# Kernel optimization log

Hardware: AMD Instinct MI355X
Metric: run time of the kernel (lower is better)

## Reference

```python
import jax, jax.numpy as jnp
import numpy as np

B, T, C = 2, 4096, 768
N_HEAD = 12
HEAD_DIM = C // N_HEAD


def setup_inputs() -> dict:
    key = jax.random.key(0)
    k1, k2, k3, k4, k5 = jax.random.split(key, 5)
    scale = 1.0 / np.sqrt(C)
    x = jax.random.normal(k1, (B, T, C), dtype=jnp.float32)
    # weights stored as [in, out] (transpose of torch Linear weight)
    W_attn = jax.random.normal(k2, (C, 3 * C), dtype=jnp.float32) * scale
    b_attn = jax.random.normal(k3, (3 * C,), dtype=jnp.float32) * 0.01
    W_proj = jax.random.normal(k4, (C, C), dtype=jnp.float32) * scale
    b_proj = jax.random.normal(k5, (C,), dtype=jnp.float32) * 0.01
    return {"x": x, "W_attn": W_attn, "b_attn": b_attn, "W_proj": W_proj, "b_proj": b_proj}


def reference(x, W_attn, b_attn, W_proj, b_proj):
    Bq, Tq, Cq = x.shape
    qkv = x @ W_attn + b_attn                      # [B, T, 3C]
    q, k, v = jnp.split(qkv, 3, axis=-1)           # each [B, T, C]

    def heads(t):
        return t.reshape(Bq, Tq, N_HEAD, HEAD_DIM).transpose(0, 2, 1, 3)  # [B, H, T, D]

    q, k, v = heads(q), heads(k), heads(v)
    att = jnp.einsum('bhqd,bhkd->bhqk', q, k) * (1.0 / np.sqrt(HEAD_DIM))  # [B, H, T, T]
    causal = jnp.tril(jnp.ones((Tq, Tq), dtype=bool))                      # [T, T]
    att = jnp.where(causal[None, None], att, jnp.finfo(att.dtype).min)
    att = jax.nn.softmax(att, axis=-1)
    y = jnp.einsum('bhqk,bhkd->bhqd', att, v)      # [B, H, T, D]
    y = y.transpose(0, 2, 1, 3).reshape(Bq, Tq, Cq)
    return y @ W_proj + b_proj
```

## Files before the change

### kernel.cpp

```cpp
#include <hip/hip_runtime.h>


#define TSEQ   4096
#define NHEAD  12
#define CDIM   768
#define C3     2304
#define BT_TOT 8192

#define PSTR   72

typedef __bf16 bf16x8 __attribute__((ext_vector_type(8)));
typedef float  f32x4  __attribute__((ext_vector_type(4)));

__device__ __forceinline__ unsigned short f2bf(float f) {
  unsigned int u = __builtin_bit_cast(unsigned int, f);
  u += 0x7FFFu + ((u >> 16) & 1u);
  return (unsigned short)(u >> 16);
}

__device__ __forceinline__ unsigned int pack2bf(float a, float b) {
  return (unsigned int)f2bf(a) | ((unsigned int)f2bf(b) << 16);
}

__device__ __forceinline__ f32x4 mfma16(bf16x8 a, bf16x8 b, f32x4 c) {
  return __builtin_amdgcn_mfma_f32_16x16x32_bf16(a, b, c, 0, 0, 0);
}

typedef const __attribute__((address_space(1))) void* gas_ptr;
typedef __attribute__((address_space(3))) void* las_ptr;

#define LGKM_WAIT() __builtin_amdgcn_s_waitcnt(0xC07F)


__global__ __launch_bounds__(256) void cast_f32_bf16(const float* __restrict__ x,
                                                     unsigned short* __restrict__ o, int n) {
  int i = (blockIdx.x * 256 + threadIdx.x) * 4;
  if (i < n) {
    float4 v = *(const float4*)(x + i);
    ushort4 u;
    u.x = f2bf(v.x); u.y = f2bf(v.y); u.z = f2bf(v.z); u.w = f2bf(v.w);
    *(ushort4*)(o + i) = u;
  }
}

__global__ __launch_bounds__(256) void transpose_cast(const float* __restrict__ src,
                                                      unsigned short* __restrict__ dst,
                                                      int K, int N) {
  __shared__ float tile[32][33];
  int n0 = blockIdx.x * 32, k0 = blockIdx.y * 32;
  int tx = threadIdx.x, ty = threadIdx.y;
#pragma unroll
  for (int i = 0; i < 4; ++i)
    tile[ty + i * 8][tx] = src[(size_t)(k0 + ty + i * 8) * N + n0 + tx];
  __syncthreads();
#pragma unroll
  for (int i = 0; i < 4; ++i)
    dst[(size_t)(n0 + ty + i * 8) * K + k0 + tx] = f2bf(tile[tx][ty + i * 8]);
}


__device__ __forceinline__ void gemm_bt_mainloop(const unsigned short* __restrict__ A,
                                                 const unsigned short* __restrict__ BTm,
                                                 int K, int m0, int n0,
                                                 unsigned short* lds, f32x4 acc[4][4]) {
  const int tid = threadIdx.x;
  const int wave = tid >> 6, lane = tid & 63;
  const int quad = lane >> 4, l16 = lane & 15;
  const int wm = (wave >> 1) * 64, wn = (wave & 1) * 64;
  const int srow = tid >> 2;
  const int scol = (tid & 3) * 8;

  for (int k0 = 0; k0 < K; k0 += 32) {
    __syncthreads();
#pragma unroll
    for (int r = 0; r < 2; ++r) {
      const unsigned short* ga = A + (size_t)(m0 + r * 64 + srow) * K + k0 + scol;
      __builtin_amdgcn_global_load_lds((gas_ptr)ga,
          (las_ptr)(lds + r * 2048 + wave * 512), 16, 0, 0);
      const unsigned short* gb = BTm + (size_t)(n0 + r * 64 + srow) * K + k0 + scol;
      __builtin_amdgcn_global_load_lds((gas_ptr)gb,
          (las_ptr)(lds + 4096 + r * 2048 + wave * 512), 16, 0, 0);
    }
    __syncthreads();

    bf16x8 af[4], bfr[4];
#pragma unroll
    for (int i = 0; i < 4; ++i) {
      af[i]  = *(const bf16x8*)(lds + (wm + i * 16 + l16) * 32 + quad * 8);
      bfr[i] = *(const bf16x8*)(lds + 4096 + (wn + i * 16 + l16) * 32 + quad * 8);
    }
#pragma unroll
    for (int i = 0; i < 4; ++i)
#pragma unroll
      for (int j = 0; j < 4; ++j)
        acc[i][j] = mfma16(af[i], bfr[j], acc[i][j]);
  }
}

__global__ __launch_bounds__(256) void gemm_qkv_kernel(
    const unsigned short* __restrict__ A, const unsigned short* __restrict__ BTm,
    const float* __restrict__ bias,
    unsigned short* __restrict__ qbuf, unsigned short* __restrict__ kbuf,
    unsigned short* __restrict__ vtbuf) {
  __shared__ __align__(16) unsigned short lds[8192];
  f32x4 zero = {0.f, 0.f, 0.f, 0.f};
  f32x4 acc[4][4];
#pragma unroll
  for (int i = 0; i < 4; ++i)
#pragma unroll
    for (int j = 0; j < 4; ++j) acc[i][j] = zero;

  const int m0 = blockIdx.y * 128, n0 = blockIdx.x * 128;
  gemm_bt_mainloop(A, BTm, CDIM, m0, n0, lds, acc);

  const int tid = threadIdx.x;
  const int wave = tid >> 6, lane = tid & 63;
  const int quad = lane >> 4, l16 = lane & 15;
  const int wm = (wave >> 1) * 64, wn = (wave & 1) * 64;
  const float KSCALE = 0.125f * 1.44269504088896340736f;

#pragma unroll
  for (int j = 0; j < 4; ++j) {
    int n = n0 + wn + j * 16 + l16;
    float bv = bias[n];
    int seg = n / CDIM;
    int nn = n - seg * CDIM;
    int h = nn >> 6, d = nn & 63;
    float mult = (seg == 1) ? KSCALE : 1.0f;
#pragma unroll
    for (int i = 0; i < 4; ++i) {
#pragma unroll
      for (int r = 0; r < 4; ++r) {
        int m = m0 + wm + i * 16 + quad * 4 + r;
        int b = m >> 12, t = m & (TSEQ - 1);
        unsigned short val = f2bf((acc[i][j][r] + bv) * mult);
        size_t bh = (size_t)(b * NHEAD + h);
        if (seg == 0)      qbuf[(bh * TSEQ + t) * 64 + d] = val;
        else if (seg == 1) kbuf[(bh * TSEQ + t) * 64 + d] = val;
        else               vtbuf[(bh * 64 + d) * TSEQ + t] = val;
      }
    }
  }
}

__global__ __launch_bounds__(256) void gemm_out_kernel(
    const unsigned short* __restrict__ A, const unsigned short* __restrict__ BTm,
    const float* __restrict__ bias, float* __restrict__ out) {
  __shared__ __align__(16) unsigned short lds[8192];
  f32x4 zero = {0.f, 0.f, 0.f, 0.f};
  f32x4 acc[4][4];
#pragma unroll
  for (int i = 0; i < 4; ++i)
#pragma unroll
    for (int j = 0; j < 4; ++j) acc[i][j] = zero;

  const int m0 = blockIdx.y * 128, n0 = blockIdx.x * 128;
  gemm_bt_mainloop(A, BTm, CDIM, m0, n0, lds, acc);

  const int tid = threadIdx.x;
  const int wave = tid >> 6, lane = tid & 63;
  const int quad = lane >> 4, l16 = lane & 15;
  const int wm = (wave >> 1) * 64, wn = (wave & 1) * 64;

#pragma unroll
  for (int j = 0; j < 4; ++j) {
    int n = n0 + wn + j * 16 + l16;
    float bv = bias[n];
#pragma unroll
    for (int i = 0; i < 4; ++i) {
#pragma unroll
      for (int r = 0; r < 4; ++r) {
        int m = m0 + wm + i * 16 + quad * 4 + r;
        out[(size_t)m * CDIM + n] = acc[i][j][r] + bv;
      }
    }
  }
}


__device__ __forceinline__ void stage_kv4(const unsigned short* __restrict__ Kp,
                                          const unsigned short* __restrict__ Vp,
                                          int j0, unsigned short* kb, unsigned short* vb,
                                          int tid, int wave) {
  const int row = tid >> 3;
  const int col = ((tid & 7) ^ (row & 7)) * 8;
  __builtin_amdgcn_global_load_lds((gas_ptr)(Kp + (size_t)(j0 + row) * 64 + col),
                                   (las_ptr)(kb + wave * 512), 16, 0, 0);
  __builtin_amdgcn_global_load_lds((gas_ptr)(Kp + (size_t)(j0 + 32 + row) * 64 + col),
                                   (las_ptr)(kb + 2048 + wave * 512), 16, 0, 0);
  __builtin_amdgcn_global_load_lds((gas_ptr)(Vp + (size_t)row * TSEQ + j0 + col),
                                   (las_ptr)(vb + wave * 512), 16, 0, 0);
  __builtin_amdgcn_global_load_lds((gas_ptr)(Vp + (size_t)(row + 32) * TSEQ + j0 + col),
                                   (las_ptr)(vb + 2048 + wave * 512), 16, 0, 0);
}

__device__ __forceinline__ void qk_score(const bf16x8 kf[8], const bf16x8 qf[2], f32x4 s[4]) {
  f32x4 zero = {0.f, 0.f, 0.f, 0.f};
#pragma unroll
  for (int i = 0; i < 4; ++i)
    s[i] = mfma16(kf[2 * i + 1], qf[1], mfma16(kf[2 * i], qf[0], zero));
}

template <bool MASKED>
__device__ __forceinline__ void exp_write(const f32x4 s[4], unsigned short* __restrict__ prow,
                                          int j0, int q0, int l16, int quad, float& lsum) {
#pragma unroll
  for (int i = 0; i < 4; ++i) {
    float p[4];
#pragma unroll
    for (int r = 0; r < 4; ++r) {
      p[r] = __builtin_amdgcn_exp2f(s[i][r]);
      if (MASKED) {
        if (j0 + i * 16 + quad * 4 + r > q0 + l16) p[r] = 0.f;
      }
      lsum += p[r];
    }
    uint2 w;
    w.x = pack2bf(p[0], p[1]);
    w.y = pack2bf(p[2], p[3]);
    *(uint2*)(prow + l16 * PSTR + i * 16 + quad * 4) = w;
  }
}

__global__ __launch_bounds__(256) void attn_kernel(const unsigned short* __restrict__ qbuf,
                                                   const unsigned short* __restrict__ kbuf,
                                                   const unsigned short* __restrict__ vtbuf,
                                                   unsigned short* __restrict__ y) {
  __shared__ __align__(16) unsigned short k_lds[2][64 * 64];
  __shared__ __align__(16) unsigned short v_lds[2][64 * 64];
  __shared__ __align__(16) unsigned short p_lds[4][16 * PSTR];

  const int tid = threadIdx.x;
  const int wave = tid >> 6, lane = tid & 63;
  const int quad = lane >> 4, l16 = lane & 15;

  const int bh = blockIdx.x % 24;
  const int qtile = 63 - (blockIdx.x / 24);
  const int q0 = qtile * 64 + wave * 16;

  const unsigned short* Qp = qbuf + (size_t)bh * TSEQ * 64;
  const unsigned short* Kp = kbuf + (size_t)bh * TSEQ * 64;
  const unsigned short* Vp = vtbuf + (size_t)bh * 64 * TSEQ;
  unsigned short* prow = &p_lds[wave][0];

  bf16x8 qf[2];
  qf[0] = *(const bf16x8*)(Qp + (size_t)(q0 + l16) * 64 + quad * 8);
  qf[1] = *(const bf16x8*)(Qp + (size_t)(q0 + l16) * 64 + 32 + quad * 8);

  f32x4 zero = {0.f, 0.f, 0.f, 0.f};
  f32x4 o[4];
#pragma unroll
  for (int dt = 0; dt < 4; ++dt) o[dt] = zero;
  float lsum = 0.f;

  const int kcol0 = (quad ^ (l16 & 7)) * 8;
  const int ntiles = qtile + 1;

  stage_kv4(Kp, Vp, 0, k_lds[0], v_lds[0], tid, wave);

  for (int jt = 0; jt < ntiles; ++jt) {
    __syncthreads();
    if (jt + 1 < ntiles)
      stage_kv4(Kp, Vp, (jt + 1) * 64, k_lds[(jt + 1) & 1], v_lds[(jt + 1) & 1], tid, wave);

    const unsigned short* kb = k_lds[jt & 1];
    const unsigned short* vb = v_lds[jt & 1];

    bf16x8 kf[8];
#pragma unroll
    for (int i = 0; i < 4; ++i) {
      kf[2 * i]     = *(const bf16x8*)(kb + (16 * i + l16) * 64 + kcol0);
      kf[2 * i + 1] = *(const bf16x8*)(kb + (16 * i + l16) * 64 + (kcol0 ^ 32));
    }
    f32x4 s[4];
    qk_score(kf, qf, s);

    if (jt == qtile) exp_write<true>(s, prow, jt * 64, q0, l16, quad, lsum);
    else             exp_write<false>(s, prow, jt * 64, q0, l16, quad, lsum);

    LGKM_WAIT();
    bf16x8 pf0 = *(const bf16x8*)(prow + l16 * PSTR + quad * 8);
    bf16x8 pf1 = *(const bf16x8*)(prow + l16 * PSTR + 32 + quad * 8);

    bf16x8 vf[8];
#pragma unroll
    for (int dt = 0; dt < 4; ++dt) {
      vf[2 * dt]     = *(const bf16x8*)(vb + (16 * dt + l16) * 64 + kcol0);
      vf[2 * dt + 1] = *(const bf16x8*)(vb + (16 * dt + l16) * 64 + (kcol0 ^ 32));
    }
#pragma unroll
    for (int dt = 0; dt < 4; ++dt)
      o[dt] = mfma16(pf1, vf[2 * dt + 1], mfma16(pf0, vf[2 * dt], o[dt]));
  }

  lsum += __shfl_xor(lsum, 16);
  lsum += __shfl_xor(lsum, 32);

  const int b = bh / NHEAD, h = bh - b * NHEAD;
#pragma unroll
  for (int r = 0; r < 4; ++r) {
    int qrow = quad * 4 + r;
    float lq = __shfl(lsum, (lane & 48) + qrow);
    float inv = 1.0f / lq;
    int t = q0 + qrow;
    size_t rowoff = (size_t)(b * TSEQ + t) * CDIM + h * 64;
#pragma unroll
    for (int dt = 0; dt < 4; ++dt)
      y[rowoff + dt * 16 + l16] = f2bf(o[dt][r] * inv);
  }
}


extern "C" void kernel_launch(void* const* d_in, const int* in_sizes, int n_in,
                              void* d_out, int out_size, void* d_ws, size_t ws_size,
                              hipStream_t stream) {
  const float* x      = (const float*)d_in[0];
  const float* W_attn = (const float*)d_in[1];
  const float* b_attn = (const float*)d_in[2];
  const float* W_proj = (const float*)d_in[3];
  const float* b_proj = (const float*)d_in[4];
  float* out = (float*)d_out;

  unsigned short* xb    = (unsigned short*)d_ws;
  unsigned short* WaT   = xb + (size_t)BT_TOT * CDIM;
  unsigned short* WpT   = WaT + (size_t)C3 * CDIM;
  unsigned short* qbuf  = WpT + (size_t)CDIM * CDIM;
  unsigned short* kbuf  = qbuf + (size_t)2 * NHEAD * TSEQ * 64;
  unsigned short* vtbuf = kbuf + (size_t)2 * NHEAD * TSEQ * 64;
  unsigned short* ybuf  = xb;

  cast_f32_bf16<<<(BT_TOT * CDIM) / 1024, 256, 0, stream>>>(x, xb, BT_TOT * CDIM);
  transpose_cast<<<dim3(C3 / 32, CDIM / 32), dim3(32, 8), 0, stream>>>(W_attn, WaT, CDIM, C3);
  transpose_cast<<<dim3(CDIM / 32, CDIM / 32), dim3(32, 8), 0, stream>>>(W_proj, WpT, CDIM, CDIM);

  gemm_qkv_kernel<<<dim3(C3 / 128, BT_TOT / 128), 256, 0, stream>>>(xb, WaT, b_attn,
                                                                    qbuf, kbuf, vtbuf);
  attn_kernel<<<dim3(2 * NHEAD * (TSEQ / 64)), 256, 0, stream>>>(qbuf, kbuf, vtbuf, ybuf);
  gemm_out_kernel<<<dim3(CDIM / 128, BT_TOT / 128), 256, 0, stream>>>(ybuf, WpT, b_proj, out);
}
```

Baseline: 266.0 us.

## Widen attention query tile to 128 and stage QKV epilogue through LDS

Result: faster. 254.0 us (-4.5%).

```diff
diff --git a/kernel.cpp b/kernel.cpp
--- a/kernel.cpp
+++ b/kernel.cpp
@@ -10,6 +10,7 @@
 #define PSTR   72
 
 typedef __bf16 bf16x8 __attribute__((ext_vector_type(8)));
+typedef __bf16 bf16x2 __attribute__((ext_vector_type(2)));
 typedef float  f32x4  __attribute__((ext_vector_type(4)));
 
 __device__ __forceinline__ unsigned short f2bf(float f) {
@@ -19,7 +20,8 @@
 }
 
 __device__ __forceinline__ unsigned int pack2bf(float a, float b) {
-  return (unsigned int)f2bf(a) | ((unsigned int)f2bf(b) << 16);
+  bf16x2 v = {(__bf16)a, (__bf16)b};
+  return __builtin_bit_cast(unsigned int, v);
 }
 
 __device__ __forceinline__ f32x4 mfma16(bf16x8 a, bf16x8 b, f32x4 c) {
@@ -102,7 +104,7 @@
     const float* __restrict__ bias,
     unsigned short* __restrict__ qbuf, unsigned short* __restrict__ kbuf,
     unsigned short* __restrict__ vtbuf) {
-  __shared__ __align__(16) unsigned short lds[8192];
+  __shared__ __align__(16) unsigned short lds[128 * 136];
   f32x4 zero = {0.f, 0.f, 0.f, 0.f};
   f32x4 acc[4][4];
 #pragma unroll
@@ -119,28 +121,45 @@
   const int wm = (wave >> 1) * 64, wn = (wave & 1) * 64;
   const float KSCALE = 0.125f * 1.44269504088896340736f;
 
+  const int seg = n0 / CDIM;
+  const float mult = (seg == 1) ? KSCALE : 1.0f;
+
+  __syncthreads();
 #pragma unroll
   for (int j = 0; j < 4; ++j) {
-    int n = n0 + wn + j * 16 + l16;
-    float bv = bias[n];
-    int seg = n / CDIM;
-    int nn = n - seg * CDIM;
-    int h = nn >> 6, d = nn & 63;
-    float mult = (seg == 1) ? KSCALE : 1.0f;
+    const int nl = wn + j * 16 + l16;
+    const float bv = bias[n0 + nl];
 #pragma unroll
     for (int i = 0; i < 4; ++i) {
 #pragma unroll
       for (int r = 0; r < 4; ++r) {
-        int m = m0 + wm + i * 16 + quad * 4 + r;
-        int b = m >> 12, t = m & (TSEQ - 1);
+        const int ml = wm + i * 16 + quad * 4 + r;
         unsigned short val = f2bf((acc[i][j][r] + bv) * mult);
-        size_t bh = (size_t)(b * NHEAD + h);
-        if (seg == 0)      qbuf[(bh * TSEQ + t) * 64 + d] = val;
-        else if (seg == 1) kbuf[(bh * TSEQ + t) * 64 + d] = val;
-        else               vtbuf[(bh * 64 + d) * TSEQ + t] = val;
+        if (seg < 2) lds[ml * 136 + nl] = val;
+        else         lds[nl * 136 + ml] = val;
       }
     }
   }
+  __syncthreads();
+
+  const int row = tid >> 1, half = tid & 1;
+  const unsigned short* src = lds + row * 136 + half * 64;
+  unsigned short* dst;
+  if (seg < 2) {
+    const int m = m0 + row, b = m >> 12, t = m & (TSEQ - 1);
+    const int nn = (n0 - seg * CDIM) + half * 64;
+    const int h = nn >> 6;
+    unsigned short* base = (seg == 0) ? qbuf : kbuf;
+    dst = base + ((size_t)(b * NHEAD + h) * TSEQ + t) * 64;
+  } else {
+    const int nn = (n0 - 2 * CDIM) + row;
+    const int h = nn >> 6, d = nn & 63;
+    const int b = m0 >> 12, t0 = (m0 & (TSEQ - 1)) + half * 64;
+    dst = vtbuf + ((size_t)(b * NHEAD + h) * 64 + d) * TSEQ + t0;
+  }
+#pragma unroll
+  for (int k = 0; k < 8; ++k)
+    *(uint4*)(dst + k * 8) = *(const uint4*)(src + k * 8);
 }
 
 __global__ __launch_bounds__(256) void gemm_out_kernel(
@@ -222,39 +241,56 @@
   }
 }
 
-__global__ __launch_bounds__(256) void attn_kernel(const unsigned short* __restrict__ qbuf,
-                                                   const unsigned short* __restrict__ kbuf,
-                                                   const unsigned short* __restrict__ vtbuf,
-                                                   unsigned short* __restrict__ y) {
+__device__ __forceinline__ void pv8(const unsigned short* __restrict__ vb, int kcol0,
+                                    const unsigned short* __restrict__ prow,
+                                    int l16, int quad, f32x4 o[4]) {
+  bf16x8 pf0 = *(const bf16x8*)(prow + l16 * PSTR + quad * 8);
+  bf16x8 pf1 = *(const bf16x8*)(prow + l16 * PSTR + 32 + quad * 8);
+#pragma unroll
+  for (int dt = 0; dt < 4; ++dt) {
+    bf16x8 v0 = *(const bf16x8*)(vb + (16 * dt + l16) * 64 + kcol0);
+    bf16x8 v1 = *(const bf16x8*)(vb + (16 * dt + l16) * 64 + (kcol0 ^ 32));
+    o[dt] = mfma16(pf1, v1, mfma16(pf0, v0, o[dt]));
+  }
+}
+
+__global__ __launch_bounds__(256, 3) void attn_kernel(const unsigned short* __restrict__ qbuf,
+                                                      const unsigned short* __restrict__ kbuf,
+                                                      const unsigned short* __restrict__ vtbuf,
+                                                      unsigned short* __restrict__ y) {
   __shared__ __align__(16) unsigned short k_lds[2][64 * 64];
   __shared__ __align__(16) unsigned short v_lds[2][64 * 64];
-  __shared__ __align__(16) unsigned short p_lds[4][16 * PSTR];
+  __shared__ __align__(16) unsigned short p_lds[4][2][16 * PSTR];
 
   const int tid = threadIdx.x;
   const int wave = tid >> 6, lane = tid & 63;
   const int quad = lane >> 4, l16 = lane & 15;
 
   const int bh = blockIdx.x % 24;
-  const int qtile = 63 - (blockIdx.x / 24);
-  const int q0 = qtile * 64 + wave * 16;
+  const int qblk = 31 - (blockIdx.x / 24);
+  const int qA0 = qblk * 128 + wave * 32;
+  const int qB0 = qA0 + 16;
 
   const unsigned short* Qp = qbuf + (size_t)bh * TSEQ * 64;
   const unsigned short* Kp = kbuf + (size_t)bh * TSEQ * 64;
   const unsigned short* Vp = vtbuf + (size_t)bh * 64 * TSEQ;
-  unsigned short* prow = &p_lds[wave][0];
-
-  bf16x8 qf[2];
-  qf[0] = *(const bf16x8*)(Qp + (size_t)(q0 + l16) * 64 + quad * 8);
-  qf[1] = *(const bf16x8*)(Qp + (size_t)(q0 + l16) * 64 + 32 + quad * 8);
+  unsigned short* prowA = &p_lds[wave][0][0];
+  unsigned short* prowB = &p_lds[wave][1][0];
+
+  bf16x8 qfA[2], qfB[2];
+  qfA[0] = *(const bf16x8*)(Qp + (size_t)(qA0 + l16) * 64 + quad * 8);
+  qfA[1] = *(const bf16x8*)(Qp + (size_t)(qA0 + l16) * 64 + 32 + quad * 8);
+  qfB[0] = *(const bf16x8*)(Qp + (size_t)(qB0 + l16) * 64 + quad * 8);
+  qfB[1] = *(const bf16x8*)(Qp + (size_t)(qB0 + l16) * 64 + 32 + quad * 8);
 
   f32x4 zero = {0.f, 0.f, 0.f, 0.f};
-  f32x4 o[4];
-#pragma unroll
-  for (int dt = 0; dt < 4; ++dt) o[dt] = zero;
-  float lsum = 0.f;
+  f32x4 oA[4], oB[4];
+#pragma unroll
+  for (int dt = 0; dt < 4; ++dt) { oA[dt] = zero; oB[dt] = zero; }
+  float lsA = 0.f, lsB = 0.f;
 
   const int kcol0 = (quad ^ (l16 & 7)) * 8;
-  const int ntiles = qtile + 1;
+  const int ntiles = 2 * qblk + 2;
 
   stage_kv4(Kp, Vp, 0, k_lds[0], v_lds[0], tid, wave);
 
@@ -265,6 +301,9 @@
 
     const unsigned short* kb = k_lds[jt & 1];
     const unsigned short* vb = v_lds[jt & 1];
+    const int j0 = jt * 64;
+    const bool anyA = j0 <= qA0 + 15;
+    const bool anyB = j0 <= qB0 + 15;
 
     bf16x8 kf[8];
 #pragma unroll
@@ -272,41 +311,39 @@
       kf[2 * i]     = *(const bf16x8*)(kb + (16 * i + l16) * 64 + kcol0);
       kf[2 * i + 1] = *(const bf16x8*)(kb + (16 * i + l16) * 64 + (kcol0 ^ 32));
     }
-    f32x4 s[4];
-    qk_score(kf, qf, s);
-
-    if (jt == qtile) exp_write<true>(s, prow, jt * 64, q0, l16, quad, lsum);
-    else             exp_write<false>(s, prow, jt * 64, q0, l16, quad, lsum);
+
+    f32x4 sA[4], sB[4];
+    qk_score(kf, qfA, sA);
+    qk_score(kf, qfB, sB);
+
+    if (j0 + 63 <= qA0)      exp_write<false>(sA, prowA, j0, qA0, l16, quad, lsA);
+    else if (anyA)           exp_write<true>(sA, prowA, j0, qA0, l16, quad, lsA);
+    if (j0 + 63 <= qB0)      exp_write<false>(sB, prowB, j0, qB0, l16, quad, lsB);
+    else if (anyB)           exp_write<true>(sB, prowB, j0, qB0, l16, quad, lsB);
 
     LGKM_WAIT();
-    bf16x8 pf0 = *(const bf16x8*)(prow + l16 * PSTR + quad * 8);
-    bf16x8 pf1 = *(const bf16x8*)(prow + l16 * PSTR + 32 + quad * 8);
-
-    bf16x8 vf[8];
+
+    if (anyA) pv8(vb, kcol0, prowA, l16, quad, oA);
+    if (anyB) pv8(vb, kcol0, prowB, l16, quad, oB);
+  }
+
+  lsA += __shfl_xor(lsA, 16); lsA += __shfl_xor(lsA, 32);
+  lsB += __shfl_xor(lsB, 16); lsB += __shfl_xor(lsB, 32);
+
+  const int b = bh / NHEAD, h = bh - b * NHEAD;
+#pragma unroll
+  for (int r = 0; r < 4; ++r) {
+    const int qrow = quad * 4 + r;
+    float lqA = __shfl(lsA, (lane & 48) + qrow);
+    float lqB = __shfl(lsB, (lane & 48) + qrow);
+    float invA = 1.0f / lqA, invB = 1.0f / lqB;
+    size_t rowA = (size_t)(b * TSEQ + qA0 + qrow) * CDIM + h * 64;
+    size_t rowB = (size_t)(b * TSEQ + qB0 + qrow) * CDIM + h * 64;
 #pragma unroll
     for (int dt = 0; dt < 4; ++dt) {
-      vf[2 * dt]     = *(const bf16x8*)(vb + (16 * dt + l16) * 64 + kcol0);
-      vf[2 * dt + 1] = *(const bf16x8*)(vb + (16 * dt + l16) * 64 + (kcol0 ^ 32));
-    }
-#pragma unroll
-    for (int dt = 0; dt < 4; ++dt)
-      o[dt] = mfma16(pf1, vf[2 * dt + 1], mfma16(pf0, vf[2 * dt], o[dt]));
-  }
-
-  lsum += __shfl_xor(lsum, 16);
-  lsum += __shfl_xor(lsum, 32);
-
-  const int b = bh / NHEAD, h = bh - b * NHEAD;
-#pragma unroll
-  for (int r = 0; r < 4; ++r) {
-    int qrow = quad * 4 + r;
-    float lq = __shfl(lsum, (lane & 48) + qrow);
-    float inv = 1.0f / lq;
-    int t = q0 + qrow;
-    size_t rowoff = (size_t)(b * TSEQ + t) * CDIM + h * 64;
-#pragma unroll
-    for (int dt = 0; dt < 4; ++dt)
-      y[rowoff + dt * 16 + l16] = f2bf(o[dt][r] * inv);
+      y[rowA + dt * 16 + l16] = f2bf(oA[dt][r] * invA);
+      y[rowB + dt * 16 + l16] = f2bf(oB[dt][r] * invB);
+    }
   }
 }
 
@@ -335,6 +372,6 @@
 
   gemm_qkv_kernel<<<dim3(C3 / 128, BT_TOT / 128), 256, 0, stream>>>(xb, WaT, b_attn,
                                                                     qbuf, kbuf, vtbuf);
-  attn_kernel<<<dim3(2 * NHEAD * (TSEQ / 64)), 256, 0, stream>>>(qbuf, kbuf, vtbuf, ybuf);
+  attn_kernel<<<dim3(2 * NHEAD * (TSEQ / 128)), 256, 0, stream>>>(qbuf, kbuf, vtbuf, ybuf);
   gemm_out_kernel<<<dim3(CDIM / 128, BT_TOT / 128), 256, 0, stream>>>(ybuf, WpT, b_proj, out);
 }
```
